# Optimization experiments

Measured on AMD Instinct MI355X. Metric: run time of the kernel, lower is better.

Reference implementation:

```python
import jax, jax.numpy as jnp
import numpy as np

SIZE = 256
D_IN = 256
EPS = 1e-3  # keras BatchNormalization default epsilon


def _mlp(x, W1, b1, W2, b2):
    # smallMLP: Dense(size, relu) -> Dense(size)
    return jax.nn.relu(x @ W1 + b1) @ W2 + b2


def setup_inputs() -> dict:
    key = jax.random.key(0)
    ks = jax.random.split(key, 20)
    B, L1, L2 = 16, 1024, 1024
    s = 0.02
    inp = {
        "seq1M": jax.random.normal(ks[0], (B, L1, D_IN), jnp.float32),
        "seq2M": jax.random.normal(ks[1], (B, L2, D_IN), jnp.float32),
        "distogram": jax.random.uniform(ks[2], (B, L1, L2), jnp.float32),
        # shared K/Q/V smallMLP params (same layers applied to seq1 and seq2)
        "kW1": jax.random.normal(ks[3], (D_IN, SIZE), jnp.float32) * s,
        "kb1": jnp.zeros((SIZE,), jnp.float32),
        "kW2": jax.random.normal(ks[4], (SIZE, SIZE), jnp.float32) * s,
        "kb2": jnp.zeros((SIZE,), jnp.float32),
        "qW1": jax.random.normal(ks[5], (D_IN, SIZE), jnp.float32) * s,
        "qb1": jnp.zeros((SIZE,), jnp.float32),
        "qW2": jax.random.normal(ks[6], (SIZE, SIZE), jnp.float32) * s,
        "qb2": jnp.zeros((SIZE,), jnp.float32),
        "vW1": jax.random.normal(ks[7], (D_IN, SIZE), jnp.float32) * s,
        "vb1": jnp.zeros((SIZE,), jnp.float32),
        "vW2": jax.random.normal(ks[8], (SIZE, SIZE), jnp.float32) * s,
        "vb2": jnp.zeros((SIZE,), jnp.float32),
        # output projections
        "fc1W": jax.random.normal(ks[9], (SIZE, SIZE), jnp.float32) * s,
        "fc1b": jnp.zeros((SIZE,), jnp.float32),
        "fc2W": jax.random.normal(ks[10], (SIZE, SIZE), jnp.float32) * s,
        "fc2b": jnp.zeros((SIZE,), jnp.float32),
        # shared BatchNorm (inference mode, moving stats)
        "bn_gamma": jnp.ones((SIZE,), jnp.float32),
        "bn_beta": jnp.zeros((SIZE,), jnp.float32),
        "bn_mean": jnp.zeros((SIZE,), jnp.float32),
        "bn_var": jnp.ones((SIZE,), jnp.float32),
    }
    return inp


def reference(seq1M, seq2M, distogram,
              kW1, kb1, kW2, kb2,
              qW1, qb1, qW2, qb2,
              vW1, vb1, vW2, vb2,
              fc1W, fc1b, fc2W, fc2b,
              bn_gamma, bn_beta, bn_mean, bn_var):
    size = jnp.float32(SIZE)
    k1 = _mlp(seq1M, kW1, kb1, kW2, kb2)   # [B, L1, S]
    q1 = _mlp(seq1M, qW1, qb1, qW2, qb2)
    v1 = _mlp(seq1M, vW1, vb1, vW2, vb2)
    k2 = _mlp(seq2M, kW1, kb1, kW2, kb2)   # [B, L2, S]
    q2 = _mlp(seq2M, qW1, qb1, qW2, qb2)
    v2 = _mlp(seq2M, vW1, vb1, vW2, vb2)

    # distogram-scaled scores, softmax over axis 1 (query axis — non-standard)
    scores1 = jnp.einsum('bls,bms->blm', q1, k2) * distogram / size  # [B, L1, L2]
    w1 = jax.nn.softmax(scores1, axis=1)
    scores2 = jnp.einsum('bms,bls->bml', q2, k1) * jnp.transpose(distogram, (0, 2, 1)) / size  # [B, L2, L1]
    w2 = jax.nn.softmax(scores2, axis=1)

    # transpose(matmul(V^T, W), [0,2,1]) == einsum contracting the softmax axis
    ap1 = jnp.einsum('bls,blm->bms', v1, w1)  # [B, L2, S]
    ap2 = jnp.einsum('bms,bml->bls', v2, w2)  # [B, L1, S]

    def bn(x):
        return (x - bn_mean) * jax.lax.rsqrt(bn_var + EPS) * bn_gamma + bn_beta

    out1 = bn(jax.nn.relu(ap1 @ fc1W + fc1b))
    out2 = bn(jax.nn.relu(ap2 @ fc2W + fc2b))
    return out1, out2
```

## Files before the change

### kernel.cpp

```cpp
#include <hip/hip_runtime.h>
#include <hip/hip_bf16.h>


typedef __attribute__((ext_vector_type(8))) short bf16x8;
typedef __attribute__((ext_vector_type(4))) float f32x4;
typedef unsigned short u16;

__device__ __forceinline__ unsigned int f2bfbits(float f) {
  union { float f; unsigned int i; } v; v.f = f;
  return (v.i + 0x7fffu + ((v.i >> 16) & 1u)) >> 16;
}
__device__ __forceinline__ unsigned int pk2(float a, float b) {
  return f2bfbits(a) | (f2bfbits(b) << 16);
}
__device__ __forceinline__ float bf2f(u16 x) {
  union { unsigned int i; float f; } v;
  v.i = (unsigned int)x << 16;
  return v.f;
}

__global__ void pack_wt(const float* __restrict__ w0, const float* __restrict__ w1,
                        const float* __restrict__ w2, const float* __restrict__ w3,
                        const float* __restrict__ w4, const float* __restrict__ w5,
                        const float* __restrict__ w6, const float* __restrict__ w7,
                        u16* __restrict__ out) {
  const float* wsel[8] = {w0, w1, w2, w3, w4, w5, w6, w7};
  const float* W = wsel[blockIdx.y];
  u16* o = out + (size_t)blockIdx.y * 65536;
  int i0 = blockIdx.x * 1024 + threadIdx.x * 4;
  int n = i0 >> 8, k = i0 & 255;
  float a = W[(k + 0) * 256 + n];
  float b = W[(k + 1) * 256 + n];
  float c = W[(k + 2) * 256 + n];
  float d = W[(k + 3) * 256 + n];
  uint2 pv;
  pv.x = pk2(a, b);
  pv.y = pk2(c, d);
  *(uint2*)(o + i0) = pv;
}

__global__ __launch_bounds__(256, 2)
void mlp3_plus(const float* __restrict__ seqA, const float* __restrict__ seqB,
               const u16* __restrict__ Wt8,
               const float* __restrict__ kb1, const float* __restrict__ kb2,
               const float* __restrict__ qb1, const float* __restrict__ qb2,
               const float* __restrict__ vb1, const float* __restrict__ vb2,
               u16* __restrict__ kA, u16* __restrict__ qA, u16* __restrict__ vA,
               u16* __restrict__ kB, u16* __restrict__ qB, u16* __restrict__ vB,
               const float* __restrict__ D, u16* __restrict__ Dt)
{
  __shared__ union {
    struct {
      u16 As[64][256];
      u16 Hl[64][256];
    } m;
    u16 T[64][72];
  } sh;

  const int tid = threadIdx.x;

  if (blockIdx.x >= 512) {
    const int pb = blockIdx.x - 512;
    const int m0 = (pb & 15) * 64;
    const int l0 = ((pb >> 4) & 15) * 64;
    const int b = pb >> 8;
    const float* src = D + (size_t)b * (1024 * 1024);
    u16* dst = Dt + (size_t)b * (1024 * 1024);
    const int r = tid >> 2, c0 = (tid & 3) * 16;
    float4 f[4];
#pragma unroll
    for (int q = 0; q < 4; ++q)
      f[q] = *(const float4*)(src + (size_t)(l0 + r) * 1024 + m0 + c0 + q * 4);
    uint4 p0, p1;
    p0.x = pk2(f[0].x, f[0].y); p0.y = pk2(f[0].z, f[0].w);
    p0.z = pk2(f[1].x, f[1].y); p0.w = pk2(f[1].z, f[1].w);
    p1.x = pk2(f[2].x, f[2].y); p1.y = pk2(f[2].z, f[2].w);
    p1.z = pk2(f[3].x, f[3].y); p1.w = pk2(f[3].z, f[3].w);
    *(uint4*)&sh.T[r][c0] = p0;
    *(uint4*)&sh.T[r][c0 + 8] = p1;
    __syncthreads();
    u16 vals[16];
#pragma unroll
    for (int k = 0; k < 16; ++k) vals[k] = sh.T[c0 + k][r];
    *(uint4*)(dst + (size_t)(m0 + r) * 1024 + l0 + c0) = *(uint4*)&vals[0];
    *(uint4*)(dst + (size_t)(m0 + r) * 1024 + l0 + c0 + 8) = *(uint4*)&vals[8];
    return;
  }

  const int lane = tid & 63;
  const int w = tid >> 6;
  const int l15 = lane & 15, lq = lane >> 4;
  const int seqsel = blockIdx.x >> 8;
  const size_t m0 = (size_t)(blockIdx.x & 255) * 64;
  const float* __restrict__ seq = seqsel ? seqB : seqA;

  {
    const int row = tid >> 2, cg = tid & 3;
    const float* src = seq + (m0 + row) * 256 + cg * 64;
#pragma unroll
    for (int cc = 0; cc < 8; ++cc) {
      float4 f0 = *(const float4*)(src + cc * 8);
      float4 f1 = *(const float4*)(src + cc * 8 + 4);
      uint4 pk;
      pk.x = pk2(f0.x, f0.y);
      pk.y = pk2(f0.z, f0.w);
      pk.z = pk2(f1.x, f1.y);
      pk.w = pk2(f1.z, f1.w);
      const int ch = (cg * 8 + cc) ^ (row & 7);
      *(uint4*)&sh.m.As[row][ch * 8] = pk;
    }
  }
  __syncthreads();

  for (int mlp = 0; mlp < 3; ++mlp) {
    const u16* __restrict__ W1 = Wt8 + (size_t)(mlp * 2) * 65536;
    const u16* __restrict__ W2 = W1 + 65536;
    const float* __restrict__ b1 = (mlp == 0) ? kb1 : (mlp == 1) ? qb1 : vb1;
    const float* __restrict__ b2 = (mlp == 0) ? kb2 : (mlp == 1) ? qb2 : vb2;
    u16* __restrict__ dst =
        (mlp == 0) ? (seqsel ? kB : kA) : (mlp == 1) ? (seqsel ? qB : qA) : (seqsel ? vB : vA);

    const u16* __restrict__ w1b = W1 + (size_t)(w * 64 + l15) * 256 + lq * 8;
    const u16* __restrict__ w2b = W2 + (size_t)(w * 64 + l15) * 256 + lq * 8;

    bf16x8 wf[3][4];
#pragma unroll
    for (int ni = 0; ni < 4; ++ni) wf[0][ni] = *(const bf16x8*)(w1b + ni * 4096);
#pragma unroll
    for (int ni = 0; ni < 4; ++ni) wf[1][ni] = *(const bf16x8*)(w1b + ni * 4096 + 32);

    float b1v[4][4];
#pragma unroll
    for (int ni = 0; ni < 4; ++ni)
#pragma unroll
      for (int r = 0; r < 4; ++r) b1v[ni][r] = b1[w * 64 + ni * 16 + 4 * lq + r];
    float b2v[4];
#pragma unroll
    for (int ni = 0; ni < 4; ++ni) b2v[ni] = b2[w * 64 + ni * 16 + l15];

    f32x4 a1[4][4];
#pragma unroll
    for (int ni = 0; ni < 4; ++ni)
#pragma unroll
      for (int mj = 0; mj < 4; ++mj) a1[ni][mj] = (f32x4)0.0f;
#pragma unroll
    for (int ks = 0; ks < 8; ++ks) {
      if (ks + 2 < 8) {
#pragma unroll
        for (int ni = 0; ni < 4; ++ni)
          wf[(ks + 2) % 3][ni] = *(const bf16x8*)(w1b + ni * 4096 + (ks + 2) * 32);
      }
      bf16x8 af[4];
#pragma unroll
      for (int mj = 0; mj < 4; ++mj) {
        const int row = mj * 16 + l15;
        const int ch = (ks * 4 + lq) ^ (row & 7);
        af[mj] = *(const bf16x8*)&sh.m.As[row][ch * 8];
      }
#pragma unroll
      for (int ni = 0; ni < 4; ++ni)
#pragma unroll
        for (int mj = 0; mj < 4; ++mj)
          a1[ni][mj] = __builtin_amdgcn_mfma_f32_16x16x32_bf16(
              wf[ks % 3][ni], af[mj], a1[ni][mj], 0, 0, 0);
    }

    __syncthreads();

#pragma unroll
    for (int ni = 0; ni < 4; ++ni) wf[0][ni] = *(const bf16x8*)(w2b + ni * 4096);
#pragma unroll
    for (int ni = 0; ni < 4; ++ni) wf[1][ni] = *(const bf16x8*)(w2b + ni * 4096 + 32);

#pragma unroll
    for (int ni = 0; ni < 4; ++ni) {
      const int chl = w * 8 + ni * 2 + (lq >> 1);
#pragma unroll
      for (int mj = 0; mj < 4; ++mj) {
        const int m = mj * 16 + l15;
        float h0 = fmaxf(a1[ni][mj][0] + b1v[ni][0], 0.f);
        float h1 = fmaxf(a1[ni][mj][1] + b1v[ni][1], 0.f);
        float h2 = fmaxf(a1[ni][mj][2] + b1v[ni][2], 0.f);
        float h3 = fmaxf(a1[ni][mj][3] + b1v[ni][3], 0.f);
        uint2 pv;
        pv.x = pk2(h0, h1);
        pv.y = pk2(h2, h3);
        const int ch = chl ^ (m & 7);
        *(uint2*)&sh.m.Hl[m][ch * 8 + (lq & 1) * 4] = pv;
      }
    }
    __syncthreads();

    f32x4 a2[4][4];
#pragma unroll
    for (int mi = 0; mi < 4; ++mi)
#pragma unroll
      for (int ni = 0; ni < 4; ++ni) a2[mi][ni] = (f32x4)0.0f;
#pragma unroll
    for (int ks = 0; ks < 8; ++ks) {
      if (ks + 2 < 8) {
#pragma unroll
        for (int ni = 0; ni < 4; ++ni)
          wf[(ks + 2) % 3][ni] = *(const bf16x8*)(w2b + ni * 4096 + (ks + 2) * 32);
      }
      bf16x8 hf[4];
#pragma unroll
      for (int mi = 0; mi < 4; ++mi) {
        const int row = mi * 16 + l15;
        const int ch = (ks * 4 + lq) ^ (row & 7);
        hf[mi] = *(const bf16x8*)&sh.m.Hl[row][ch * 8];
      }
#pragma unroll
      for (int mi = 0; mi < 4; ++mi)
#pragma unroll
        for (int ni = 0; ni < 4; ++ni)
          a2[mi][ni] = __builtin_amdgcn_mfma_f32_16x16x32_bf16(
              hf[mi], wf[ks % 3][ni], a2[mi][ni], 0, 0, 0);
    }

#pragma unroll
    for (int ni = 0; ni < 4; ++ni) {
      const int col = w * 64 + ni * 16 + l15;
      const float bb = b2v[ni];
#pragma unroll
      for (int mi = 0; mi < 4; ++mi) {
        const size_t grow0 = m0 + mi * 16 + 4 * lq;
        float z[4];
#pragma unroll
        for (int r = 0; r < 4; ++r) z[r] = a2[mi][ni][r] + bb;
        if (mlp != 2) {
#pragma unroll
          for (int r = 0; r < 4; ++r)
            dst[(grow0 + r) * 256 + col] = (u16)f2bfbits(z[r]);
        } else {
          uint2 pv;
          pv.x = pk2(z[0], z[1]);
          pv.y = pk2(z[2], z[3]);
          const size_t bb2 = grow0 >> 10, lrow = grow0 & 1023;
          *(uint2*)(dst + ((size_t)bb2 * 256 + col) * 1024 + lrow) = pv;
        }
      }
    }
  }
}

__global__ __launch_bounds__(256, 2)
void gemm_bn2(const u16* __restrict__ ap1, const u16* __restrict__ ap2,
              const u16* __restrict__ Wt8,
              const float* __restrict__ fc1b, const float* __restrict__ fc2b,
              float* __restrict__ out1, float* __restrict__ out2,
              const float* __restrict__ bn_g, const float* __restrict__ bn_b,
              const float* __restrict__ bn_m, const float* __restrict__ bn_v)
{
  __shared__ u16 As[128][64];
  __shared__ u16 Ws[64][64];
  const int tid = threadIdx.x;
  const int lane = tid & 63;
  const int w = tid >> 6;
  const int wr = w >> 1, wc = w & 1;
  const int l15 = lane & 15, lq = lane >> 4;
  const size_t bm = (size_t)blockIdx.x * 128;
  const int bn = blockIdx.y * 64;
  const int which = blockIdx.z;

  const u16* __restrict__ A0 = which ? ap2 : ap1;
  const u16* __restrict__ Wt = Wt8 + (size_t)(6 + which) * 65536;
  const float* __restrict__ bias = which ? fc2b : fc1b;
  float* __restrict__ Cout = which ? out2 : out1;

  const int sar = tid >> 1, sah = tid & 1;
  const int swr = tid >> 2, swc = tid & 3;

  f32x4 acc[4][2];
#pragma unroll
  for (int mi = 0; mi < 4; ++mi)
#pragma unroll
    for (int ni = 0; ni < 2; ++ni) acc[mi][ni] = (f32x4)0.0f;

  for (int k0 = 0; k0 < 256; k0 += 64) {
    __syncthreads();
    {
      const u16* A = A0 + (bm + sar) * 256 + k0 + sah * 32;
#pragma unroll
      for (int c = 0; c < 4; ++c) {
        uint4 v = *(const uint4*)(A + c * 8);
        int cc = (sah * 4 + c) ^ (sar & 7);
        *(uint4*)&As[sar][cc * 8] = v;
      }
    }
    {
      const u16* Wp = Wt + (size_t)(bn + swr) * 256 + k0 + swc * 16;
#pragma unroll
      for (int c = 0; c < 2; ++c) {
        uint4 v = *(const uint4*)(Wp + c * 8);
        int cc = (swc * 2 + c) ^ (swr & 7);
        *(uint4*)&Ws[swr][cc * 8] = v;
      }
    }
    __syncthreads();
#pragma unroll
    for (int ks = 0; ks < 2; ++ks) {
      bf16x8 af[4], wf[2];
#pragma unroll
      for (int mi = 0; mi < 4; ++mi) {
        int row = wr * 64 + mi * 16 + l15;
        int cc = (ks * 4 + lq) ^ (row & 7);
        af[mi] = *(const bf16x8*)&As[row][cc * 8];
      }
#pragma unroll
      for (int ni = 0; ni < 2; ++ni) {
        int row = wc * 32 + ni * 16 + l15;
        int cc = (ks * 4 + lq) ^ (row & 7);
        wf[ni] = *(const bf16x8*)&Ws[row][cc * 8];
      }
#pragma unroll
      for (int mi = 0; mi < 4; ++mi)
#pragma unroll
        for (int ni = 0; ni < 2; ++ni)
          acc[mi][ni] = __builtin_amdgcn_mfma_f32_16x16x32_bf16(
              af[mi], wf[ni], acc[mi][ni], 0, 0, 0);
    }
  }

#pragma unroll
  for (int ni = 0; ni < 2; ++ni) {
    const int col = bn + wc * 32 + ni * 16 + l15;
    const float bi = bias[col];
    const float g = bn_g[col];
    const float be = bn_b[col];
    const float mu = bn_m[col];
    const float iv = rsqrtf(bn_v[col] + 1e-3f);
#pragma unroll
    for (int mi = 0; mi < 4; ++mi) {
      const size_t grow0 = bm + wr * 64 + mi * 16 + 4 * lq;
#pragma unroll
      for (int r = 0; r < 4; ++r) {
        float z = acc[mi][ni][r] + bi;
        float zz = fmaxf(z, 0.f);
        Cout[(grow0 + r) * 256 + col] = (zz - mu) * iv * g + be;
      }
    }
  }
}

__global__ __launch_bounds__(256, 2)
void attn_mfma(const u16* __restrict__ Qa, const u16* __restrict__ Ka,
               const u16* __restrict__ Va, u16* __restrict__ OutA,
               const u16* __restrict__ Qb, const u16* __restrict__ Kb,
               const u16* __restrict__ Vb, u16* __restrict__ OutB,
               const u16* __restrict__ D1t, const float* __restrict__ D2)
{
  __shared__ union U {
    struct {
      u16 Ks[2][32][256];
      u16 Vts[256][32];
      u16 Pl[64][40];
    } s;
    u16 Osw[4][16][264];
  } u;

  const int orig = blockIdx.x;
  const int lid = (orig & 7) * 64 + (orig >> 3);
  const int dir = lid >> 8;
  const int b = (lid >> 4) & 15;
  const int i0 = (lid & 15) * 64;

  const u16* __restrict__ Q = dir ? Qb : Qa;
  const u16* __restrict__ K = dir ? Kb : Ka;
  const u16* __restrict__ Vt = dir ? Vb : Va;
  u16* __restrict__ Out = dir ? OutB : OutA;

  const int tid = threadIdx.x;
  const int lane = tid & 63;
  const int w = tid >> 6;
  const int l15 = lane & 15, lq = lane >> 4;
  const size_t sbase = (size_t)b * (1024 * 256);
  const size_t vtbase = (size_t)b * (256 * 1024);
  const size_t dbase = (size_t)b * (1024 * 1024);

  bf16x8 q[8];
  {
    const u16* Qp = Q + sbase + (size_t)(i0 + w * 16 + l15) * 256 + lq * 8;
#pragma unroll
    for (int ks = 0; ks < 8; ++ks) q[ks] = *(const bf16x8*)(Qp + ks * 32);
  }

  const int cb0 = w * 4;
  auto stage_K = [&](int bi, int j0) {
#pragma unroll
    for (int i = 0; i < 4; ++i) {
      const int cb = cb0 + i;
      const int krow = cb * 2 + (lane >> 5);
      const int kch = (lane & 31) ^ (krow & 7);
      const u16* gs = K + sbase + (size_t)(j0 + krow) * 256 + kch * 8;
      __builtin_amdgcn_global_load_lds(
          (const __attribute__((address_space(1))) unsigned int*)gs,
          (__attribute__((address_space(3))) unsigned int*)&u.s.Ks[bi][cb * 2][0],
          16, 0, 0);
    }
  };
  auto stage_V = [&](int j0) {
#pragma unroll
    for (int i = 0; i < 4; ++i) {
      const int cb = cb0 + i;
      const int vrow = cb * 16 + (lane >> 2);
      const int vch = lane & 3;
      const u16* gs = Vt + vtbase + (size_t)vrow * 1024 + j0 + ((vch ^ (vrow & 3)) * 8);
      __builtin_amdgcn_global_load_lds(
          (const __attribute__((address_space(1))) unsigned int*)gs,
          (__attribute__((address_space(3))) unsigned int*)&u.s.Vts[cb * 16][0],
          16, 0, 0);
    }
  };

  float mrow[4], lsum[4];
  f32x4 o[16];
#pragma unroll
  for (int r = 0; r < 4; ++r) { mrow[r] = -1e30f; lsum[r] = 0.f; }
#pragma unroll
  for (int nt = 0; nt < 16; ++nt) o[nt] = (f32x4)0.0f;

  stage_K(0, 0);

  const int vcc = lq ^ (l15 & 3);

  for (int t = 0; t < 32; ++t) {
    const int bi = t & 1;
    const int j0 = t * 32;

    u16 bregu[8];
    float bregf[8];
    if (dir == 0) {
#pragma unroll
      for (int nt = 0; nt < 2; ++nt)
#pragma unroll
        for (int r = 0; r < 4; ++r)
          bregu[nt * 4 + r] =
              D1t[dbase + (size_t)(i0 + w * 16 + 4 * lq + r) * 1024 + j0 + l15 + 16 * nt];
    } else {
#pragma unroll
      for (int nt = 0; nt < 2; ++nt)
#pragma unroll
        for (int r = 0; r < 4; ++r)
          bregf[nt * 4 + r] =
              D2[dbase + (size_t)(i0 + w * 16 + 4 * lq + r) * 1024 + j0 + l15 + 16 * nt];
    }

    stage_V(j0);
    __builtin_amdgcn_sched_barrier(0);
    if (t + 1 < 32) {
      stage_K(bi ^ 1, j0 + 32);
      asm volatile("s_waitcnt vmcnt(16)" ::: "memory");
    } else {
      asm volatile("s_waitcnt vmcnt(12)" ::: "memory");
    }
    __builtin_amdgcn_s_barrier();
    __builtin_amdgcn_sched_barrier(0);

    f32x4 sa[2];
    sa[0] = (f32x4)0.0f;
    sa[1] = (f32x4)0.0f;
    __builtin_amdgcn_s_setprio(1);
#pragma unroll
    for (int ks = 0; ks < 8; ++ks)
#pragma unroll
      for (int nt = 0; nt < 2; ++nt) {
        const int row = nt * 16 + l15;
        const int cc = (ks * 4 + lq) ^ (row & 7);
        bf16x8 kb = *(const bf16x8*)&u.s.Ks[bi][row][cc * 8];
        sa[nt] = __builtin_amdgcn_mfma_f32_16x16x32_bf16(q[ks], kb, sa[nt], 0, 0, 0);
      }
    __builtin_amdgcn_s_setprio(0);

    float s0[4], s1[4];
    bool need = false;
#pragma unroll
    for (int r = 0; r < 4; ++r) {
      const float b0 = (dir == 0) ? bf2f(bregu[r]) : bregf[r];
      const float b1 = (dir == 0) ? bf2f(bregu[4 + r]) : bregf[4 + r];
      s0[r] = sa[0][r] * b0 * 0.00390625f;
      s1[r] = sa[1][r] * b1 * 0.00390625f;
      need = need || (s0[r] > mrow[r] + 8.f) || (s1[r] > mrow[r] + 8.f);
    }
    if (__any(need)) {
#pragma unroll
      for (int r = 0; r < 4; ++r) {
        float mx = fmaxf(s0[r], s1[r]);
        mx = fmaxf(mx, __shfl_xor(mx, 1, 16));
        mx = fmaxf(mx, __shfl_xor(mx, 2, 16));
        mx = fmaxf(mx, __shfl_xor(mx, 4, 16));
        mx = fmaxf(mx, __shfl_xor(mx, 8, 16));
        const float mn = fmaxf(mrow[r], mx);
        const float sc = __expf(mrow[r] - mn);
        mrow[r] = mn;
        lsum[r] *= sc;
#pragma unroll
        for (int nt = 0; nt < 16; ++nt) o[nt][r] *= sc;
      }
    }
    float p0v[4], p1v[4];
#pragma unroll
    for (int r = 0; r < 4; ++r) {
      p0v[r] = __expf(s0[r] - mrow[r]);
      p1v[r] = __expf(s1[r] - mrow[r]);
      lsum[r] += p0v[r] + p1v[r];
    }
#pragma unroll
    for (int r = 0; r < 4; ++r) {
      const int qrow = w * 16 + 4 * lq + r;
      u.s.Pl[qrow][l15] = (u16)f2bfbits(p0v[r]);
      u.s.Pl[qrow][16 + l15] = (u16)f2bfbits(p1v[r]);
    }
    if (t + 1 < 32)
      asm volatile("s_waitcnt vmcnt(4) lgkmcnt(0)" ::: "memory");
    else
      asm volatile("s_waitcnt vmcnt(0) lgkmcnt(0)" ::: "memory");
    __builtin_amdgcn_sched_barrier(0);
    __builtin_amdgcn_s_barrier();
    const bf16x8 pa = *(const bf16x8*)&u.s.Pl[w * 16 + l15][lq * 8];

    __builtin_amdgcn_s_setprio(1);
#pragma unroll
    for (int nt = 0; nt < 16; ++nt) {
      bf16x8 vb = *(const bf16x8*)&u.s.Vts[nt * 16 + l15][vcc * 8];
      o[nt] = __builtin_amdgcn_mfma_f32_16x16x32_bf16(pa, vb, o[nt], 0, 0, 0);
    }
    __builtin_amdgcn_s_setprio(0);

    asm volatile("s_waitcnt lgkmcnt(0)" ::: "memory");
    __builtin_amdgcn_s_barrier();
  }

  float inv[4];
#pragma unroll
  for (int r = 0; r < 4; ++r) {
    float rs = lsum[r];
    rs += __shfl_xor(rs, 1, 16);
    rs += __shfl_xor(rs, 2, 16);
    rs += __shfl_xor(rs, 4, 16);
    rs += __shfl_xor(rs, 8, 16);
    inv[r] = 1.0f / rs;
  }
#pragma unroll
  for (int nt = 0; nt < 16; ++nt) {
#pragma unroll
    for (int r = 0; r < 4; ++r)
      u.Osw[w][4 * lq + r][nt * 16 + l15] = (u16)f2bfbits(o[nt][r] * inv[r]);
  }
  asm volatile("s_waitcnt lgkmcnt(0)" ::: "memory");
  __builtin_amdgcn_sched_barrier(0);
  {
    const int orow = lane >> 2, och = (lane & 3) * 64;
    const u16* src = &u.Osw[w][orow][och];
    u16* dst = Out + sbase + (size_t)(i0 + w * 16 + orow) * 256 + och;
#pragma unroll
    for (int c = 0; c < 8; ++c) *(uint4*)(dst + c * 8) = *(const uint4*)(src + c * 8);
  }
}

extern "C" void kernel_launch(void* const* d_in, const int* in_sizes, int n_in,
                              void* d_out, int out_size, void* d_ws, size_t ws_size,
                              hipStream_t stream)
{
  (void)in_sizes; (void)n_in; (void)out_size; (void)ws_size;

  const float* seq1  = (const float*)d_in[0];
  const float* seq2  = (const float*)d_in[1];
  const float* disto = (const float*)d_in[2];
  const float* kW1 = (const float*)d_in[3];
  const float* kb1 = (const float*)d_in[4];
  const float* kW2 = (const float*)d_in[5];
  const float* kb2 = (const float*)d_in[6];
  const float* qW1 = (const float*)d_in[7];
  const float* qb1 = (const float*)d_in[8];
  const float* qW2 = (const float*)d_in[9];
  const float* qb2 = (const float*)d_in[10];
  const float* vW1 = (const float*)d_in[11];
  const float* vb1 = (const float*)d_in[12];
  const float* vW2 = (const float*)d_in[13];
  const float* vb2 = (const float*)d_in[14];
  const float* fc1W = (const float*)d_in[15];
  const float* fc1b = (const float*)d_in[16];
  const float* fc2W = (const float*)d_in[17];
  const float* fc2b = (const float*)d_in[18];
  const float* bn_g = (const float*)d_in[19];
  const float* bn_b = (const float*)d_in[20];
  const float* bn_m = (const float*)d_in[21];
  const float* bn_v = (const float*)d_in[22];

  char* ws = (char*)d_ws;
  const size_t MB = 1024 * 1024;
  u16* Wt8 = (u16*)(ws);
  u16* k1  = (u16*)(ws + 1 * MB);
  u16* q1  = (u16*)(ws + 9 * MB);
  u16* k2  = (u16*)(ws + 17 * MB);
  u16* q2  = (u16*)(ws + 25 * MB);
  u16* v1t = (u16*)(ws + 33 * MB);
  u16* v2t = (u16*)(ws + 41 * MB);
  u16* ap1 = (u16*)(ws + 49 * MB);
  u16* ap2 = (u16*)(ws + 57 * MB);
  u16* D1t = (u16*)(ws + 65 * MB);

  pack_wt<<<dim3(64, 8), 256, 0, stream>>>(kW1, kW2, qW1, qW2, vW1, vW2, fc1W, fc2W, Wt8);

  mlp3_plus<<<dim3(4608), dim3(256), 0, stream>>>(
      seq1, seq2, Wt8, kb1, kb2, qb1, qb2, vb1, vb2,
      k1, q1, v1t, k2, q2, v2t, disto, D1t);

  attn_mfma<<<dim3(512), dim3(256), 0, stream>>>(
      k2, q1, v1t, ap1,
      k1, q2, v2t, ap2,
      D1t, disto);

  float* out1 = (float*)d_out;
  float* out2 = (float*)d_out + 4194304;
  gemm_bn2<<<dim3(128, 4, 2), dim3(256), 0, stream>>>(
      ap1, ap2, Wt8, fc1b, fc2b, out1, out2, bn_g, bn_b, bn_m, bn_v);
}
```

Baseline: 164.3 us.

## Enlarge attention tiles to 128 query rows and 64-key steps with double-buffered V

The attention kernel now runs 8 waves per block, each block covering 128 query rows, and advances over keys in 64-wide tiles instead of 32. K and V tiles are double-buffered in LDS and prefetched one step ahead, so each staged K/V tile is reused by twice as many queries and the loop needs half as many barrier rounds. One barrier before the P read is removed because each wave only reads back its own P rows; a barrier is added before the output staging because that buffer overlaps the K/V storage. The cost is about 146 KB of LDS per block, allowing only one block per CU with a single 256-block grid, and more registers for distogram values and scores.

Result: no change. 161.3 us (median of 2 runs) (-1.8%).

```diff
diff --git a/kernel.cpp b/kernel.cpp
--- a/kernel.cpp
+++ b/kernel.cpp
@@ -343,7 +343,7 @@
   }
 }
 
-__global__ __launch_bounds__(256, 2)
+__global__ __launch_bounds__(512, 2)
 void attn_mfma(const u16* __restrict__ Qa, const u16* __restrict__ Ka,
                const u16* __restrict__ Va, u16* __restrict__ OutA,
                const u16* __restrict__ Qb, const u16* __restrict__ Kb,
@@ -352,18 +352,18 @@
 {
   __shared__ union U {
     struct {
-      u16 Ks[2][32][256];
-      u16 Vts[256][32];
-      u16 Pl[64][40];
+      u16 Ks[2][64][256];
+      u16 Vts[2][256][64];
+      u16 Pl[128][72];
     } s;
-    u16 Osw[4][16][264];
+    u16 Osw[8][16][264];
   } u;
 
   const int orig = blockIdx.x;
-  const int lid = (orig & 7) * 64 + (orig >> 3);
-  const int dir = lid >> 8;
-  const int b = (lid >> 4) & 15;
-  const int i0 = (lid & 15) * 64;
+  const int lid = (orig & 7) * 32 + (orig >> 3);
+  const int dir = lid >> 7;
+  const int b = (lid >> 3) & 15;
+  const int i0 = (lid & 7) * 128;
 
   const u16* __restrict__ Q = dir ? Qb : Qa;
   const u16* __restrict__ K = dir ? Kb : Ka;
@@ -399,16 +399,16 @@
           16, 0, 0);
     }
   };
-  auto stage_V = [&](int j0) {
+  auto stage_V = [&](int bi, int j0) {
 #pragma unroll
     for (int i = 0; i < 4; ++i) {
       const int cb = cb0 + i;
-      const int vrow = cb * 16 + (lane >> 2);
-      const int vch = lane & 3;
-      const u16* gs = Vt + vtbase + (size_t)vrow * 1024 + j0 + ((vch ^ (vrow & 3)) * 8);
+      const int vrow = cb * 8 + (lane >> 3);
+      const int vch = lane & 7;
+      const u16* gs = Vt + vtbase + (size_t)vrow * 1024 + j0 + ((vch ^ (vrow & 7)) * 8);
       __builtin_amdgcn_global_load_lds(
           (const __attribute__((address_space(1))) unsigned int*)gs,
-          (__attribute__((address_space(3))) unsigned int*)&u.s.Vts[cb * 16][0],
+          (__attribute__((address_space(3))) unsigned int*)&u.s.Vts[bi][cb * 8][0],
           16, 0, 0);
     }
   };
@@ -421,50 +421,48 @@
   for (int nt = 0; nt < 16; ++nt) o[nt] = (f32x4)0.0f;
 
   stage_K(0, 0);
-
-  const int vcc = lq ^ (l15 & 3);
-
-  for (int t = 0; t < 32; ++t) {
+  stage_V(0, 0);
+
+  for (int t = 0; t < 16; ++t) {
     const int bi = t & 1;
-    const int j0 = t * 32;
-
-    u16 bregu[8];
-    float bregf[8];
+    const int j0 = t * 64;
+
+    u16 bregu[16];
+    float bregf[16];
     if (dir == 0) {
 #pragma unroll
-      for (int nt = 0; nt < 2; ++nt)
+      for (int nt = 0; nt < 4; ++nt)
 #pragma unroll
         for (int r = 0; r < 4; ++r)
           bregu[nt * 4 + r] =
               D1t[dbase + (size_t)(i0 + w * 16 + 4 * lq + r) * 1024 + j0 + l15 + 16 * nt];
     } else {
 #pragma unroll
-      for (int nt = 0; nt < 2; ++nt)
+      for (int nt = 0; nt < 4; ++nt)
 #pragma unroll
         for (int r = 0; r < 4; ++r)
           bregf[nt * 4 + r] =
               D2[dbase + (size_t)(i0 + w * 16 + 4 * lq + r) * 1024 + j0 + l15 + 16 * nt];
     }
 
-    stage_V(j0);
-    __builtin_amdgcn_sched_barrier(0);
-    if (t + 1 < 32) {
-      stage_K(bi ^ 1, j0 + 32);
+    if (t + 1 < 16) {
+      stage_V(bi ^ 1, j0 + 64);
+      stage_K(bi ^ 1, j0 + 64);
+      asm volatile("s_waitcnt vmcnt(24)" ::: "memory");
+    } else {
       asm volatile("s_waitcnt vmcnt(16)" ::: "memory");
-    } else {
-      asm volatile("s_waitcnt vmcnt(12)" ::: "memory");
     }
     __builtin_amdgcn_s_barrier();
     __builtin_amdgcn_sched_barrier(0);
 
-    f32x4 sa[2];
-    sa[0] = (f32x4)0.0f;
-    sa[1] = (f32x4)0.0f;
+    f32x4 sa[4];
+#pragma unroll
+    for (int nt = 0; nt < 4; ++nt) sa[nt] = (f32x4)0.0f;
     __builtin_amdgcn_s_setprio(1);
 #pragma unroll
     for (int ks = 0; ks < 8; ++ks)
 #pragma unroll
-      for (int nt = 0; nt < 2; ++nt) {
+      for (int nt = 0; nt < 4; ++nt) {
         const int row = nt * 16 + l15;
         const int cc = (ks * 4 + lq) ^ (row & 7);
         bf16x8 kb = *(const bf16x8*)&u.s.Ks[bi][row][cc * 8];
@@ -472,20 +470,20 @@
       }
     __builtin_amdgcn_s_setprio(0);
 
-    float s0[4], s1[4];
+    float s[4][4];
     bool need = false;
 #pragma unroll
-    for (int r = 0; r < 4; ++r) {
-      const float b0 = (dir == 0) ? bf2f(bregu[r]) : bregf[r];
-      const float b1 = (dir == 0) ? bf2f(bregu[4 + r]) : bregf[4 + r];
-      s0[r] = sa[0][r] * b0 * 0.00390625f;
-      s1[r] = sa[1][r] * b1 * 0.00390625f;
-      need = need || (s0[r] > mrow[r] + 8.f) || (s1[r] > mrow[r] + 8.f);
-    }
+    for (int r = 0; r < 4; ++r)
+#pragma unroll
+      for (int nt = 0; nt < 4; ++nt) {
+        const float bb = (dir == 0) ? bf2f(bregu[nt * 4 + r]) : bregf[nt * 4 + r];
+        s[r][nt] = sa[nt][r] * bb * 0.00390625f;
+        need = need || (s[r][nt] > mrow[r] + 8.f);
+      }
     if (__any(need)) {
 #pragma unroll
       for (int r = 0; r < 4; ++r) {
-        float mx = fmaxf(s0[r], s1[r]);
+        float mx = fmaxf(fmaxf(s[r][0], s[r][1]), fmaxf(s[r][2], s[r][3]));
         mx = fmaxf(mx, __shfl_xor(mx, 1, 16));
         mx = fmaxf(mx, __shfl_xor(mx, 2, 16));
         mx = fmaxf(mx, __shfl_xor(mx, 4, 16));
@@ -498,32 +496,31 @@
         for (int nt = 0; nt < 16; ++nt) o[nt][r] *= sc;
       }
     }
-    float p0v[4], p1v[4];
-#pragma unroll
-    for (int r = 0; r < 4; ++r) {
-      p0v[r] = __expf(s0[r] - mrow[r]);
-      p1v[r] = __expf(s1[r] - mrow[r]);
-      lsum[r] += p0v[r] + p1v[r];
-    }
 #pragma unroll
     for (int r = 0; r < 4; ++r) {
       const int qrow = w * 16 + 4 * lq + r;
-      u.s.Pl[qrow][l15] = (u16)f2bfbits(p0v[r]);
-      u.s.Pl[qrow][16 + l15] = (u16)f2bfbits(p1v[r]);
-    }
-    if (t + 1 < 32)
-      asm volatile("s_waitcnt vmcnt(4) lgkmcnt(0)" ::: "memory");
-    else
-      asm volatile("s_waitcnt vmcnt(0) lgkmcnt(0)" ::: "memory");
+#pragma unroll
+      for (int nt = 0; nt < 4; ++nt) {
+        const float p = __expf(s[r][nt] - mrow[r]);
+        lsum[r] += p;
+        u.s.Pl[qrow][nt * 16 + l15] = (u16)f2bfbits(p);
+      }
+    }
+    asm volatile("s_waitcnt lgkmcnt(0)" ::: "memory");
     __builtin_amdgcn_sched_barrier(0);
-    __builtin_amdgcn_s_barrier();
-    const bf16x8 pa = *(const bf16x8*)&u.s.Pl[w * 16 + l15][lq * 8];
+    const bf16x8 pa0 = *(const bf16x8*)&u.s.Pl[w * 16 + l15][lq * 8];
+    const bf16x8 pa1 = *(const bf16x8*)&u.s.Pl[w * 16 + l15][32 + lq * 8];
 
     __builtin_amdgcn_s_setprio(1);
 #pragma unroll
     for (int nt = 0; nt < 16; ++nt) {
-      bf16x8 vb = *(const bf16x8*)&u.s.Vts[nt * 16 + l15][vcc * 8];
-      o[nt] = __builtin_amdgcn_mfma_f32_16x16x32_bf16(pa, vb, o[nt], 0, 0, 0);
+      const int row = nt * 16 + l15;
+      const int cc0 = (0 * 4 + lq) ^ (row & 7);
+      const int cc1 = (1 * 4 + lq) ^ (row & 7);
+      bf16x8 vb0 = *(const bf16x8*)&u.s.Vts[bi][row][cc0 * 8];
+      bf16x8 vb1 = *(const bf16x8*)&u.s.Vts[bi][row][cc1 * 8];
+      o[nt] = __builtin_amdgcn_mfma_f32_16x16x32_bf16(pa0, vb0, o[nt], 0, 0, 0);
+      o[nt] = __builtin_amdgcn_mfma_f32_16x16x32_bf16(pa1, vb1, o[nt], 0, 0, 0);
     }
     __builtin_amdgcn_s_setprio(0);
 
@@ -541,6 +538,7 @@
     rs += __shfl_xor(rs, 8, 16);
     inv[r] = 1.0f / rs;
   }
+  __builtin_amdgcn_s_barrier();
 #pragma unroll
   for (int nt = 0; nt < 16; ++nt) {
 #pragma unroll
@@ -607,7 +605,7 @@
       seq1, seq2, Wt8, kb1, kb2, qb1, qb2, vb1, vb2,
       k1, q1, v1t, k2, q2, v2t, disto, D1t);
 
-  attn_mfma<<<dim3(512), dim3(256), 0, stream>>>(
+  attn_mfma<<<dim3(256), dim3(512), 0, stream>>>(
       k2, q1, v1t, ap1,
       k1, q2, v2t, ap2,
       D1t, disto);
```
